# Kernel tuning notes

Measured on AMD Instinct MI355X. Metric: run time of the kernel, lower is better.

The kernel has to match this reference:

```python
import jax, jax.numpy as jnp
import numpy as np

D_MODEL = 1024
NUM_HEADS = 16
WINDOW = 128
DISP = WINDOW // 2
SHIFTED = True
NEG = -9e15


def _create_mask(w):
    # 1 = keep, 0 = masked; zero top-right and bottom-left DISP blocks
    m = np.ones((w, w), dtype=np.float32)
    m[:DISP, -DISP:] = 0.0
    m[-DISP:, :DISP] = 0.0
    return jnp.asarray(m)


def setup_inputs() -> dict:
    key = jax.random.key(0)
    ks = jax.random.split(key, 5)
    b, s, d = 4, 8192, D_MODEL
    sc = 1.0 / np.sqrt(d)
    return {
        "x": jax.random.normal(ks[0], (b, s, d), jnp.float32),
        "w_qkv": jax.random.normal(ks[1], (d, 3 * d), jnp.float32) * sc,
        "b_qkv": jax.random.normal(ks[2], (3 * d,), jnp.float32) * 0.02,
        "w_o": jax.random.normal(ks[3], (d, d), jnp.float32) * sc,
        "b_o": jax.random.normal(ks[4], (d,), jnp.float32) * 0.02,
    }


def reference(x, w_qkv, b_qkv, w_o, b_o):
    b, s, d = x.shape
    h, w = NUM_HEADS, WINDOW
    d_k = d // h
    if SHIFTED:
        x = jnp.roll(x, -DISP, axis=1)
    xw = x.reshape(-1, w, d)                       # (n, w, d), n = b*s/w
    n = xw.shape[0]
    qkv = xw @ w_qkv + b_qkv                       # (n, w, 3d)
    # replicate torch rearrange 'n w (h d_k qkv) -> n h w (d_k qkv)' + chunk(3)
    qkv = qkv.reshape(n, w, h, d_k, 3)             # split (h d_k qkv)
    qkv = qkv.transpose(0, 2, 1, 3, 4).reshape(n, h, w, 3 * d_k)
    q, k, v = jnp.split(qkv, 3, axis=-1)           # each (n, h, w, d_k)
    attn = jnp.einsum('nhqd,nhkd->nhqk', q, k) / jnp.sqrt(jnp.float32(d_k))
    if SHIFTED:
        mask = _create_mask(w)                     # (w, w)
        attn = jnp.where(mask == 0, jnp.float32(NEG), attn)
    attn = jax.nn.softmax(attn, axis=-1)
    vals = jnp.einsum('nhqk,nhkd->nhqd', attn, v)  # (n, h, w, d_k)
    vals = vals.transpose(0, 2, 1, 3).reshape(n, w, d)
    out = vals @ w_o + b_o                         # (n, w, d)
    out = out.reshape(b, s, d)
    if SHIFTED:
        out = jnp.roll(out, DISP, axis=1)
    return out
```

## Files before the change

kernel.cpp:

```cpp
#include <hip/hip_runtime.h>
#include <hip/hip_bf16.h>
#include <stdint.h>

#define D_MODEL   1024
#define SEQ       8192
#define BATCH     4
#define NQKV      3072
#define HEADS     16

typedef _Float16 f16;
typedef f16   f16x8 __attribute__((ext_vector_type(8)));
typedef float f32x4 __attribute__((ext_vector_type(4)));

#define AS1 __attribute__((address_space(1)))
#define AS3 __attribute__((address_space(3)))

__device__ __forceinline__ void lds_load16(const void* g, void* l) {
  __builtin_amdgcn_global_load_lds((const AS1 void*)g, (AS3 void*)l, 16, 0, 0);
}

__global__ void cvt_weights(const float* __restrict__ wqkv,
                            const float* __restrict__ bqkv,
                            const float* __restrict__ wo,
                            f16* __restrict__ wqkvT,
                            float* __restrict__ bqkvR,
                            f16* __restrict__ woT)
{
  const int NW1 = NQKV * D_MODEL;
  const int NW2 = D_MODEL * D_MODEL;
  int i = blockIdx.x * 256 + threadIdx.x;
  if (i < NW1) {
    int c = i % NQKV, k = i / NQKV;
    int hh = c / 192, rr = c % 192;
    int t  = rr >> 6, a = rr & 63;
    int n  = t * 1024 + hh * 64 + a;
    wqkvT[(size_t)n * 1024 + k] = (f16)wqkv[i];
  } else if (i < NW1 + NW2) {
    int j = i - NW1;
    int n = j % D_MODEL, k = j / D_MODEL;
    woT[(size_t)n * 1024 + k] = (f16)wo[j];
  } else if (i < NW1 + NW2 + NQKV) {
    int c = i - NW1 - NW2;
    int hh = c / 192, rr = c % 192;
    int t  = rr >> 6, a = rr & 63;
    bqkvR[t * 1024 + hh * 64 + a] = bqkv[c];
  }
}

__global__ void cvt_x(const float* __restrict__ x, f16* __restrict__ xb)
{
  int i  = blockIdx.x * 256 + threadIdx.x;
  int r  = i >> 7;
  int c8 = i & 127;
  int bb = r >> 13, p = r & 8191;
  int sr = (bb << 13) | ((p + 64) & 8191);
  const float* src = x + (size_t)sr * 1024 + c8 * 8;
  float4 v0 = *(const float4*)(src);
  float4 v1 = *(const float4*)(src + 4);
  f16x8 o = { (f16)v0.x, (f16)v0.y, (f16)v0.z, (f16)v0.w,
              (f16)v1.x, (f16)v1.y, (f16)v1.z, (f16)v1.w };
  *(f16x8*)(xb + (size_t)r * 1024 + c8 * 8) = o;
}

#define BARX() { asm volatile("" ::: "memory"); __builtin_amdgcn_s_barrier(); \
                 __builtin_amdgcn_sched_barrier(0); }

#define LOADAx(dst,d,qm) { _Pragma("unroll") for (int mi=0;mi<4;++mi){ \
    int rr = wm*64 + mi*16 + c16; \
    const char* p = lds + (d)*65536 + (qm)*16384 + rr*128; \
    _Pragma("unroll") for (int ks=0;ks<2;++ks) \
      dst[mi][ks] = *(const f16x8*)(p + ((((ks<<2)|g4) ^ (rr&7))<<4)); } }

#define LOADBx(dst,d,qn) { _Pragma("unroll") for (int nj=0;nj<2;++nj){ \
    int rr = wn*32 + nj*16 + c16; \
    const char* p = lds + (d)*65536 + 32768 + (qn)*16384 + rr*128; \
    _Pragma("unroll") for (int ks=0;ks<2;++ks) \
      dst[nj][ks] = *(const f16x8*)(p + ((((ks<<2)|g4) ^ (rr&7))<<4)); } }

#define MFC(AR,BR,qm,qn) { __builtin_amdgcn_s_setprio(1); \
    _Pragma("unroll") for (int mi=0;mi<4;++mi) \
    _Pragma("unroll") for (int nj=0;nj<2;++nj){ \
      acc[(qm)*4+mi][(qn)*2+nj] = __builtin_amdgcn_mfma_f32_16x16x32_f16( \
          AR[mi][0], BR[nj][0], acc[(qm)*4+mi][(qn)*2+nj], 0,0,0); \
      acc[(qm)*4+mi][(qn)*2+nj] = __builtin_amdgcn_mfma_f32_16x16x32_f16( \
          AR[mi][1], BR[nj][1], acc[(qm)*4+mi][(qn)*2+nj], 0,0,0); } \
    __builtin_amdgcn_s_setprio(0); }

template<int EPI>
__global__ __launch_bounds__(512, 2)
void gemm8(const f16* __restrict__ A, const f16* __restrict__ B,
           const float* __restrict__ bias,
           f16* __restrict__ outQ, f16* __restrict__ outK,
           f16* __restrict__ outVT, float* __restrict__ outF,
           int Ntiles)
{
  __shared__ alignas(16) char lds[131072];

  int nwg  = gridDim.x;
  int work = ((int)blockIdx.x & 7) * (nwg >> 3) + ((int)blockIdx.x >> 3);
  int mt = work / Ntiles, nt = work % Ntiles;
  int m0 = mt * 256, n0 = nt * 256;

  int tid = threadIdx.x;
  int w = tid >> 6, lane = tid & 63;
  int wm = w >> 2, wn = w & 3;
  int c16 = lane & 15, g4 = lane >> 4;

  int rr0 = tid >> 3;
  int sc  = (((tid & 7) ^ ((tid >> 3) & 7)) << 4);
  const char* pA = (const char*)A + (size_t)(m0 + rr0) * 2048 + sc;
  const char* pB = (const char*)B + (size_t)(n0 + ((rr0 >> 5) << 6) + (rr0 & 31)) * 2048 + sc;
  char* dstA = lds + w * 1024;
  char* dstB = lds + 32768 + w * 1024;

  auto stageA = [&](int d, int qm, int t) {
    const char* s = pA + (size_t)(qm * 64) * 2048 + (size_t)t * 128;
    lds_load16(s,              dstA + d * 65536 + qm * 16384);
    lds_load16(s + 128 * 2048, dstA + d * 65536 + qm * 16384 + 8192);
  };
  auto stageB = [&](int d, int qn, int t) {
    const char* s = pB + (size_t)(qn * 32) * 2048 + (size_t)t * 128;
    lds_load16(s,              dstB + d * 65536 + qn * 16384);
    lds_load16(s + 128 * 2048, dstB + d * 65536 + qn * 16384 + 8192);
  };

  f32x4 acc[8][4];
#pragma unroll
  for (int i = 0; i < 8; ++i)
#pragma unroll
    for (int j = 0; j < 4; ++j)
      acc[i][j] = (f32x4){0.f, 0.f, 0.f, 0.f};
  f16x8 a0[4][2], a1[4][2], b0[2][2], b1[2][2];

  stageA(0, 0, 0); stageB(0, 0, 0); stageB(0, 1, 0); stageA(0, 1, 0);
  stageA(1, 0, 1); stageB(1, 0, 1); stageB(1, 1, 1);
  asm volatile("s_waitcnt vmcnt(6)" ::: "memory");
  BARX();

  for (int t = 0; t < 16; ++t) {
    int d = t & 1, e = d ^ 1;
    LOADAx(a0, d, 0); LOADBx(b0, d, 0);
    if (t < 15) stageA(e, 1, t + 1);
    BARX(); MFC(a0, b0, 0, 0); BARX();
    LOADBx(b1, d, 1);
    if (t < 14) stageA(d, 0, t + 2);
    BARX(); MFC(a0, b1, 0, 1); BARX();
    LOADAx(a1, d, 1);
    if (t < 14) stageB(d, 0, t + 2);
    BARX(); MFC(a1, b1, 1, 1); BARX();
    if (t < 14) {
      stageB(d, 1, t + 2);
      asm volatile("s_waitcnt vmcnt(6)" ::: "memory");
    } else if (t == 14) {
      asm volatile("s_waitcnt vmcnt(0)" ::: "memory");
    }
    BARX(); MFC(a1, b0, 1, 0); BARX();
  }

  if (EPI == 0) {
    int tt = n0 >> 10;
#pragma unroll
    for (int ai = 0; ai < 8; ++ai) {
#pragma unroll
      for (int bj = 0; bj < 4; ++bj) {
        int n  = n0 + wn * 64 + bj * 16 + c16;
        int nn = n & 1023;
        float bv = bias[n];
#pragma unroll
        for (int j = 0; j < 4; ++j) {
          int m = m0 + wm * 128 + ai * 16 + g4 * 4 + j;
          float v = acc[ai][bj][j] + bv;
          if (tt == 0) {
            outQ[(size_t)m * 1024 + nn] = (f16)v;
          } else if (tt == 1) {
            outK[(size_t)m * 1024 + nn] = (f16)v;
          } else {
            int sub = m >> 6, key = m & 63;
            int hh = nn >> 6, dk = nn & 63;
            outVT[(((size_t)(sub * 16 + hh) * 64 + dk) << 6) + key] = (f16)v;
          }
        }
      }
    }
  } else {
#pragma unroll
    for (int ai = 0; ai < 8; ++ai) {
#pragma unroll
      for (int bj = 0; bj < 4; ++bj) {
        int n = n0 + wn * 64 + bj * 16 + c16;
        float bv = bias[n];
#pragma unroll
        for (int j = 0; j < 4; ++j) {
          int m = m0 + wm * 128 + ai * 16 + g4 * 4 + j;
          int bb = m >> 13, p = m & 8191;
          int dr = (bb << 13) | ((p + 64) & 8191);
          outF[(size_t)dr * 1024 + n] = acc[ai][bj][j] + bv;
        }
      }
    }
  }
}

__global__ __launch_bounds__(64)
void attn64(const f16* __restrict__ Q, const f16* __restrict__ Kb,
            const f16* __restrict__ VT, f16* __restrict__ O)
{
  __shared__ alignas(16) char plds[8192];
  int u = blockIdx.x;
  int sub = u >> 4, hh = u & 15;
  int l = threadIdx.x;
  int c = l & 15, g = l >> 4;

  const char* Qb = (const char*)Q  + (size_t)sub * 64 * 2048 + hh * 128;
  const char* KB = (const char*)Kb + (size_t)sub * 64 * 2048 + hh * 128;
  const char* VB = (const char*)VT + (size_t)u * 8192;

  f16x8 aq[4][2], bk[4][2];
#pragma unroll
  for (int mi = 0; mi < 4; ++mi)
#pragma unroll
    for (int kb = 0; kb < 2; ++kb)
      aq[mi][kb] = *(const f16x8*)(Qb + (mi * 16 + c) * 2048 + (kb * 32 + g * 8) * 2);
#pragma unroll
  for (int nj = 0; nj < 4; ++nj)
#pragma unroll
    for (int kb = 0; kb < 2; ++kb)
      bk[nj][kb] = *(const f16x8*)(KB + (nj * 16 + c) * 2048 + (kb * 32 + g * 8) * 2);

  f32x4 s[4][4];
#pragma unroll
  for (int mi = 0; mi < 4; ++mi)
#pragma unroll
    for (int nj = 0; nj < 4; ++nj)
      s[mi][nj] = (f32x4){0.f, 0.f, 0.f, 0.f};
#pragma unroll
  for (int kb = 0; kb < 2; ++kb)
#pragma unroll
    for (int mi = 0; mi < 4; ++mi)
#pragma unroll
      for (int nj = 0; nj < 4; ++nj)
        s[mi][nj] = __builtin_amdgcn_mfma_f32_16x16x32_f16(
            aq[mi][kb], bk[nj][kb], s[mi][nj], 0, 0, 0);

  const float SM_SCALE = 0.125f * 1.44269504089f;
#pragma unroll
  for (int mi = 0; mi < 4; ++mi) {
#pragma unroll
    for (int j = 0; j < 4; ++j) {
      float v0 = s[mi][0][j], v1 = s[mi][1][j], v2 = s[mi][2][j], v3 = s[mi][3][j];
      float mx = fmaxf(fmaxf(v0, v1), fmaxf(v2, v3));
      mx = fmaxf(mx, __shfl_xor(mx, 1));
      mx = fmaxf(mx, __shfl_xor(mx, 2));
      mx = fmaxf(mx, __shfl_xor(mx, 4));
      mx = fmaxf(mx, __shfl_xor(mx, 8));
      float p0 = exp2f((v0 - mx) * SM_SCALE);
      float p1 = exp2f((v1 - mx) * SM_SCALE);
      float p2 = exp2f((v2 - mx) * SM_SCALE);
      float p3 = exp2f((v3 - mx) * SM_SCALE);
      float sm = (p0 + p1) + (p2 + p3);
      sm += __shfl_xor(sm, 1);
      sm += __shfl_xor(sm, 2);
      sm += __shfl_xor(sm, 4);
      sm += __shfl_xor(sm, 8);
      float inv = 1.0f / sm;
      int r = mi * 16 + g * 4 + j;
      int rbyte = r * 128, rx = (r & 7) << 4;
      {
        int key = c;
        *(f16*)(plds + rbyte + (((key >> 3) << 4) ^ rx) + ((key & 7) << 1)) = (f16)(p0 * inv);
      }
      {
        int key = 16 + c;
        *(f16*)(plds + rbyte + (((key >> 3) << 4) ^ rx) + ((key & 7) << 1)) = (f16)(p1 * inv);
      }
      {
        int key = 32 + c;
        *(f16*)(plds + rbyte + (((key >> 3) << 4) ^ rx) + ((key & 7) << 1)) = (f16)(p2 * inv);
      }
      {
        int key = 48 + c;
        *(f16*)(plds + rbyte + (((key >> 3) << 4) ^ rx) + ((key & 7) << 1)) = (f16)(p3 * inv);
      }
    }
  }
  __syncthreads();

  f16x8 ap[4][2], bv[4][2];
#pragma unroll
  for (int mi = 0; mi < 4; ++mi) {
    int rowq = mi * 16 + c;
    int base = rowq * 128, rx = rowq & 7;
#pragma unroll
    for (int kb = 0; kb < 2; ++kb) {
      int ch = ((kb << 2) | g) ^ rx;
      ap[mi][kb] = *(const f16x8*)(plds + base + (ch << 4));
    }
  }
#pragma unroll
  for (int nj = 0; nj < 4; ++nj) {
    int dk = nj * 16 + c;
#pragma unroll
    for (int kb = 0; kb < 2; ++kb)
      bv[nj][kb] = *(const f16x8*)(VB + (dk * 64 + kb * 32 + g * 8) * 2);
  }

  f32x4 o[4][4];
#pragma unroll
  for (int mi = 0; mi < 4; ++mi)
#pragma unroll
    for (int nj = 0; nj < 4; ++nj)
      o[mi][nj] = (f32x4){0.f, 0.f, 0.f, 0.f};
#pragma unroll
  for (int kb = 0; kb < 2; ++kb)
#pragma unroll
    for (int mi = 0; mi < 4; ++mi)
#pragma unroll
      for (int nj = 0; nj < 4; ++nj)
        o[mi][nj] = __builtin_amdgcn_mfma_f32_16x16x32_f16(
            ap[mi][kb], bv[nj][kb], o[mi][nj], 0, 0, 0);

#pragma unroll
  for (int mi = 0; mi < 4; ++mi)
#pragma unroll
    for (int nj = 0; nj < 4; ++nj)
#pragma unroll
      for (int j = 0; j < 4; ++j) {
        int qrow = mi * 16 + g * 4 + j;
        int dk = nj * 16 + c;
        O[(size_t)(sub * 64 + qrow) * 1024 + hh * 64 + dk] = (f16)o[mi][nj][j];
      }
}

extern "C" void kernel_launch(void* const* d_in, const int* in_sizes, int n_in,
                              void* d_out, int out_size, void* d_ws, size_t ws_size,
                              hipStream_t stream)
{
  const float* x    = (const float*)d_in[0];
  const float* wqkv = (const float*)d_in[1];
  const float* bqkv = (const float*)d_in[2];
  const float* wo   = (const float*)d_in[3];
  const float* bo   = (const float*)d_in[4];
  float* out = (float*)d_out;
  char* ws = (char*)d_ws;

  f16*   xb    = (f16*)(ws + 0);
  f16*   wqkvT = (f16*)(ws + 67108864);
  float* bqkvR = (float*)(ws + 73400320);
  f16*   woT   = (f16*)(ws + 73412608);
  f16*   Qb    = (f16*)(ws + 75509760);
  f16*   Kb    = (f16*)(ws + 142618624);
  f16*   VTb   = (f16*)(ws + 209727488);
  f16*   A2    = (f16*)(ws + 0);

  cvt_weights<<<16396, 256, 0, stream>>>(wqkv, bqkv, wo, wqkvT, bqkvR, woT);
  cvt_x<<<16384, 256, 0, stream>>>(x, xb);
  gemm8<0><<<1536, 512, 0, stream>>>(xb, wqkvT, bqkvR, Qb, Kb, VTb, nullptr, 12);
  attn64<<<8192, 64, 0, stream>>>(Qb, Kb, VTb, A2);
  gemm8<1><<<512, 512, 0, stream>>>(A2, woT, bo, nullptr, nullptr, nullptr, out, 4);
}
```

Baseline: 675.1 us.

## Split 256x256 GEMM tile across 16 waves with finer-grained k-step LDS loads

The GEMM kernel now runs 1024 threads (16 waves) per 256x256 tile instead of 512, halving each wave's accumulator footprint (4x4 instead of 8x4 fragments). The LDS fragment loads are split per k-substep with explicit lgkmcnt waits, and the global-to-LDS staging is regrouped so each thread issues one 16-byte load per stage. The goal is more waves in flight to hide LDS and MFMA latency and lower register pressure. In exchange it adds barrier overhead, and with 128 KB of LDS per block occupancy stays at one block per CU, so the launch_bounds hint of 4 blocks cannot be met.

```diff
diff --git a/kernel.cpp b/kernel.cpp
--- a/kernel.cpp
+++ b/kernel.cpp
@@ -63,36 +63,33 @@
 }
 
 #define BARX() { asm volatile("" ::: "memory"); __builtin_amdgcn_s_barrier(); \
-                 __builtin_amdgcn_sched_barrier(0); }
-
-#define LOADAx(dst,d,qm) { _Pragma("unroll") for (int mi=0;mi<4;++mi){ \
-    int rr = wm*64 + mi*16 + c16; \
-    const char* p = lds + (d)*65536 + (qm)*16384 + rr*128; \
-    _Pragma("unroll") for (int ks=0;ks<2;++ks) \
-      dst[mi][ks] = *(const f16x8*)(p + ((((ks<<2)|g4) ^ (rr&7))<<4)); } }
-
-#define LOADBx(dst,d,qn) { _Pragma("unroll") for (int nj=0;nj<2;++nj){ \
-    int rr = wn*32 + nj*16 + c16; \
-    const char* p = lds + (d)*65536 + 32768 + (qn)*16384 + rr*128; \
-    _Pragma("unroll") for (int ks=0;ks<2;++ks) \
-      dst[nj][ks] = *(const f16x8*)(p + ((((ks<<2)|g4) ^ (rr&7))<<4)); } }
-
-#define MFC(AR,BR,qm,qn) { __builtin_amdgcn_s_setprio(1); \
+                 asm volatile("" ::: "memory"); }
+#define LGKM0() asm volatile("s_waitcnt lgkmcnt(0)" ::: "memory");
+
+#define LOADA(d,ks) { _Pragma("unroll") for (int mi=0;mi<4;++mi){ \
+    int hr = hrA + mi*16; \
+    const char* p = lds + (d)*65536 + qmA*16384 + hr*128; \
+    af[mi] = *(const f16x8*)(p + ((((ks)<<2)|g4) ^ (hr&7))*16); } }
+
+#define LOADB(d,ks,nh) { _Pragma("unroll") for (int nj2=0;nj2<2;++nj2){ \
+    int hr = hrB + nj2*16; \
+    const char* p = lds + (d)*65536 + 32768 + (nh)*16384 + hr*128; \
+    bl[nj2] = *(const f16x8*)(p + ((((ks)<<2)|g4) ^ (hr&7))*16); } }
+
+#define MF8(nh) { __builtin_amdgcn_s_setprio(1); \
     _Pragma("unroll") for (int mi=0;mi<4;++mi) \
-    _Pragma("unroll") for (int nj=0;nj<2;++nj){ \
-      acc[(qm)*4+mi][(qn)*2+nj] = __builtin_amdgcn_mfma_f32_16x16x32_f16( \
-          AR[mi][0], BR[nj][0], acc[(qm)*4+mi][(qn)*2+nj], 0,0,0); \
-      acc[(qm)*4+mi][(qn)*2+nj] = __builtin_amdgcn_mfma_f32_16x16x32_f16( \
-          AR[mi][1], BR[nj][1], acc[(qm)*4+mi][(qn)*2+nj], 0,0,0); } \
+    _Pragma("unroll") for (int nj2=0;nj2<2;++nj2) \
+      acc[mi][(nh)*2+nj2] = __builtin_amdgcn_mfma_f32_16x16x32_f16( \
+          af[mi], bl[nj2], acc[mi][(nh)*2+nj2], 0,0,0); \
     __builtin_amdgcn_s_setprio(0); }
 
 template<int EPI>
-__global__ __launch_bounds__(512, 2)
-void gemm8(const f16* __restrict__ A, const f16* __restrict__ B,
-           const float* __restrict__ bias,
-           f16* __restrict__ outQ, f16* __restrict__ outK,
-           f16* __restrict__ outVT, float* __restrict__ outF,
-           int Ntiles)
+__global__ __launch_bounds__(1024, 4)
+void gemm16(const f16* __restrict__ A, const f16* __restrict__ B,
+            const float* __restrict__ bias,
+            f16* __restrict__ outQ, f16* __restrict__ outK,
+            f16* __restrict__ outVT, float* __restrict__ outF,
+            int Ntiles)
 {
   __shared__ alignas(16) char lds[131072];
 
@@ -105,71 +102,73 @@
   int w = tid >> 6, lane = tid & 63;
   int wm = w >> 2, wn = w & 3;
   int c16 = lane & 15, g4 = lane >> 4;
+  int qmA = wm & 1;
+  int hrA = (wm >> 1) * 64 + c16;
+  int hrB = wn * 32 + c16;
 
   int rr0 = tid >> 3;
-  int sc  = (((tid & 7) ^ ((tid >> 3) & 7)) << 4);
-  const char* pA = (const char*)A + (size_t)(m0 + rr0) * 2048 + sc;
-  const char* pB = (const char*)B + (size_t)(n0 + ((rr0 >> 5) << 6) + (rr0 & 31)) * 2048 + sc;
+  int sc  = (((tid & 7) ^ (rr0 & 7)) << 4);
+  const char* pA = (const char*)A
+      + (size_t)(m0 + (rr0 & 63) + ((rr0 >> 6) << 7)) * 2048 + sc;
+  const char* pB = (const char*)B
+      + (size_t)(n0 + (rr0 & 31) + ((rr0 >> 5) << 6)) * 2048 + sc;
   char* dstA = lds + w * 1024;
   char* dstB = lds + 32768 + w * 1024;
 
   auto stageA = [&](int d, int qm, int t) {
-    const char* s = pA + (size_t)(qm * 64) * 2048 + (size_t)t * 128;
-    lds_load16(s,              dstA + d * 65536 + qm * 16384);
-    lds_load16(s + 128 * 2048, dstA + d * 65536 + qm * 16384 + 8192);
+    lds_load16(pA + (size_t)qm * 131072 + (size_t)t * 128,
+               dstA + d * 65536 + qm * 16384);
   };
   auto stageB = [&](int d, int qn, int t) {
-    const char* s = pB + (size_t)(qn * 32) * 2048 + (size_t)t * 128;
-    lds_load16(s,              dstB + d * 65536 + qn * 16384);
-    lds_load16(s + 128 * 2048, dstB + d * 65536 + qn * 16384 + 8192);
+    lds_load16(pB + (size_t)qn * 65536 + (size_t)t * 128,
+               dstB + d * 65536 + qn * 16384);
   };
 
-  f32x4 acc[8][4];
-#pragma unroll
-  for (int i = 0; i < 8; ++i)
+  f32x4 acc[4][4];
+#pragma unroll
+  for (int i = 0; i < 4; ++i)
 #pragma unroll
     for (int j = 0; j < 4; ++j)
       acc[i][j] = (f32x4){0.f, 0.f, 0.f, 0.f};
-  f16x8 a0[4][2], a1[4][2], b0[2][2], b1[2][2];
-
-  stageA(0, 0, 0); stageB(0, 0, 0); stageB(0, 1, 0); stageA(0, 1, 0);
-  stageA(1, 0, 1); stageB(1, 0, 1); stageB(1, 1, 1);
-  asm volatile("s_waitcnt vmcnt(6)" ::: "memory");
+  f16x8 af[4], bl[2];
+
+  stageA(0, 0, 0); stageA(0, 1, 0); stageB(0, 0, 0); stageB(0, 1, 0);
+  stageA(1, 0, 1); stageB(1, 0, 1);
+  asm volatile("s_waitcnt vmcnt(2)" ::: "memory");
   BARX();
 
   for (int t = 0; t < 16; ++t) {
     int d = t & 1, e = d ^ 1;
-    LOADAx(a0, d, 0); LOADBx(b0, d, 0);
-    if (t < 15) stageA(e, 1, t + 1);
-    BARX(); MFC(a0, b0, 0, 0); BARX();
-    LOADBx(b1, d, 1);
-    if (t < 14) stageA(d, 0, t + 2);
-    BARX(); MFC(a0, b1, 0, 1); BARX();
-    LOADAx(a1, d, 1);
-    if (t < 14) stageB(d, 0, t + 2);
-    BARX(); MFC(a1, b1, 1, 1); BARX();
+    LOADA(d, 0); LOADB(d, 0, 0);
+    if (t < 15) { stageA(e, 1, t + 1); stageB(e, 1, t + 1); }
+    BARX(); LGKM0(); MF8(0); BARX();
+    LOADB(d, 0, 1);
+    BARX(); LGKM0(); MF8(1); BARX();
+    LOADA(d, 1); LOADB(d, 1, 0);
+    BARX(); LGKM0(); MF8(0); BARX();
+    LOADB(d, 1, 1);
     if (t < 14) {
-      stageB(d, 1, t + 2);
-      asm volatile("s_waitcnt vmcnt(6)" ::: "memory");
+      stageA(d, 0, t + 2); stageB(d, 0, t + 2);
+      asm volatile("s_waitcnt vmcnt(2)" ::: "memory");
     } else if (t == 14) {
       asm volatile("s_waitcnt vmcnt(0)" ::: "memory");
     }
-    BARX(); MFC(a1, b0, 1, 0); BARX();
+    BARX(); LGKM0(); MF8(1); BARX();
   }
 
   if (EPI == 0) {
     int tt = n0 >> 10;
 #pragma unroll
-    for (int ai = 0; ai < 8; ++ai) {
-#pragma unroll
-      for (int bj = 0; bj < 4; ++bj) {
-        int n  = n0 + wn * 64 + bj * 16 + c16;
+    for (int mi = 0; mi < 4; ++mi) {
+#pragma unroll
+      for (int nj = 0; nj < 4; ++nj) {
+        int n  = n0 + wn * 64 + nj * 16 + c16;
         int nn = n & 1023;
         float bv = bias[n];
 #pragma unroll
         for (int j = 0; j < 4; ++j) {
-          int m = m0 + wm * 128 + ai * 16 + g4 * 4 + j;
-          float v = acc[ai][bj][j] + bv;
+          int m = m0 + wm * 64 + mi * 16 + g4 * 4 + j;
+          float v = acc[mi][nj][j] + bv;
           if (tt == 0) {
             outQ[(size_t)m * 1024 + nn] = (f16)v;
           } else if (tt == 1) {
@@ -184,17 +183,17 @@
     }
   } else {
 #pragma unroll
-    for (int ai = 0; ai < 8; ++ai) {
-#pragma unroll
-      for (int bj = 0; bj < 4; ++bj) {
-        int n = n0 + wn * 64 + bj * 16 + c16;
+    for (int mi = 0; mi < 4; ++mi) {
+#pragma unroll
+      for (int nj = 0; nj < 4; ++nj) {
+        int n = n0 + wn * 64 + nj * 16 + c16;
         float bv = bias[n];
 #pragma unroll
         for (int j = 0; j < 4; ++j) {
-          int m = m0 + wm * 128 + ai * 16 + g4 * 4 + j;
+          int m = m0 + wm * 64 + mi * 16 + g4 * 4 + j;
           int bb = m >> 13, p = m & 8191;
           int dr = (bb << 13) | ((p + 64) & 8191);
-          outF[(size_t)dr * 1024 + n] = acc[ai][bj][j] + bv;
+          outF[(size_t)dr * 1024 + n] = acc[mi][nj][j] + bv;
         }
       }
     }
@@ -354,7 +353,7 @@
 
   cvt_weights<<<16396, 256, 0, stream>>>(wqkv, bqkv, wo, wqkvT, bqkvR, woT);
   cvt_x<<<16384, 256, 0, stream>>>(x, xb);
-  gemm8<0><<<1536, 512, 0, stream>>>(xb, wqkvT, bqkvR, Qb, Kb, VTb, nullptr, 12);
+  gemm16<0><<<1536, 1024, 0, stream>>>(xb, wqkvT, bqkvR, Qb, Kb, VTb, nullptr, 12);
   attn64<<<8192, 64, 0, stream>>>(Qb, Kb, VTb, A2);
-  gemm8<1><<<512, 512, 0, stream>>>(A2, woT, bo, nullptr, nullptr, nullptr, out, 4);
-}
+  gemm16<1><<<512, 1024, 0, stream>>>(A2, woT, bo, nullptr, nullptr, nullptr, out, 4);
+}
```

Result: no change. 664.3 us (-1.6%).
